# Kernel optimization log

Measured on AMD Instinct MI355X. Metric: run time of the kernel, lower is better.

The kernel has to match this reference:

```python
import jax, jax.numpy as jnp
import numpy as np

N_NODES = 100000
N_EDGES = 1600000
DIM = 128
N_LAYERS = 3
BN_EPS = 1e-5


def setup_inputs() -> dict:
    key = jax.random.key(0)
    ks = jax.random.split(key, 8)
    x = jax.random.normal(ks[0], (N_NODES, DIM), dtype=jnp.float32)
    edge_index = jax.random.randint(ks[1], (2, N_EDGES), 0, N_NODES, dtype=jnp.int64)
    batch = jax.random.randint(ks[2], (N_NODES,), 0, 64, dtype=jnp.int64)
    # stacked per-layer params (input_dim == hidden_dim == 128)
    W = jax.random.normal(ks[3], (N_LAYERS, DIM, DIM), dtype=jnp.float32) / np.sqrt(DIM)
    b = jnp.zeros((N_LAYERS, DIM), dtype=jnp.float32)
    gamma = jax.random.normal(ks[4], (N_LAYERS, DIM), dtype=jnp.float32) * 0.1 + 1.0
    beta = jax.random.normal(ks[5], (N_LAYERS, DIM), dtype=jnp.float32) * 0.1
    running_mean = jax.random.normal(ks[6], (N_LAYERS, DIM), dtype=jnp.float32) * 0.1
    running_var = jax.random.uniform(ks[7], (N_LAYERS, DIM), dtype=jnp.float32, minval=0.5, maxval=1.5)
    return {"x": x, "edge_index": edge_index, "batch": batch, "W": W, "b": b,
            "gamma": gamma, "beta": beta,
            "running_mean": running_mean, "running_var": running_var}


def reference(x, edge_index, batch, W, b, gamma, beta, running_mean, running_var):
    # batch is unused by the original forward (kept for signature fidelity)
    n = x.shape[0]
    # GCNConv adds self-loops once per layer; precompute augmented edge list + norm
    loops = jnp.arange(n, dtype=edge_index.dtype)
    src = jnp.concatenate([edge_index[0], loops])
    dst = jnp.concatenate([edge_index[1], loops])
    deg = jax.ops.segment_sum(jnp.ones_like(dst, dtype=x.dtype), dst, num_segments=n)
    dinv = jax.lax.rsqrt(jnp.maximum(deg, 1e-12))
    norm = dinv[src] * dinv[dst]  # [E+N]

    h = x
    for l in range(N_LAYERS):
        # GCNConv: propagate normalized messages of (h @ W), then add bias
        hw = h @ W[l]                                   # [N, D]
        msg = hw[src] * norm[:, None]                   # gather  [E+N, D]
        h = jax.ops.segment_sum(msg, dst, num_segments=n) + b[l]
        # BatchNorm1d (eval mode: running stats) + ReLU; dropout is identity in eval
        h = gamma[l] * (h - running_mean[l]) * jax.lax.rsqrt(running_var[l] + BN_EPS) + beta[l]
        h = jax.nn.relu(h)
    return h
```

## Files before the change

### kernel.cpp

```cpp
#include <hip/hip_runtime.h>

#define N_NODES 100000
#define N_EDGES 1600000
#define DIM 128
#define BN_EPS 1e-5f
#define BSHIFT 9
#define BN 512
#define NB 196
#define CAP_S 9216
#define CAP_C 10048
#define CHUNK 4096

typedef _Float16 f16;
typedef _Float16 f16x4 __attribute__((ext_vector_type(4)));
typedef _Float16 f16x8 __attribute__((ext_vector_type(8)));
typedef float f32x4 __attribute__((ext_vector_type(4)));


__global__ __launch_bounds__(256) void k_binA(const int* __restrict__ src,
                                              const int* __restrict__ dst,
                                              int* __restrict__ bcnt,
                                              int2* __restrict__ stage) {
  __shared__ int hist[NB];
  __shared__ int lofs[NB];
  __shared__ int lbase[NB];
  __shared__ int lcur[NB];
  __shared__ int scanbuf[256];
  __shared__ int2 buf[CHUNK];
  int t = threadIdx.x;
  for (int i = t; i < NB; i += 256) { hist[i] = 0; lcur[i] = 0; }
  __syncthreads();
  int e0 = blockIdx.x * CHUNK;
  int en = min(CHUNK, N_EDGES - e0);
  for (int i = t; i < en; i += 256) {
    unsigned d = (unsigned)dst[e0 + i];
    unsigned s = (unsigned)src[e0 + i];
    if (d < N_NODES && s < N_NODES) atomicAdd(&hist[d >> BSHIFT], 1);
  }
  __syncthreads();
  scanbuf[t] = (t < NB) ? hist[t] : 0;
  __syncthreads();
  for (int off = 1; off < 256; off <<= 1) {
    int x = (t >= off) ? scanbuf[t - off] : 0;
    __syncthreads();
    scanbuf[t] += x;
    __syncthreads();
  }
  if (t < NB) {
    lofs[t] = scanbuf[t] - hist[t];
    lbase[t] = atomicAdd(&bcnt[t], hist[t]);
  }
  __syncthreads();
  for (int i = t; i < en; i += 256) {
    int d = dst[e0 + i], s = src[e0 + i];
    if ((unsigned)d < N_NODES && (unsigned)s < N_NODES) {
      int b = d >> BSHIFT;
      int r = atomicAdd(&lcur[b], 1);
      buf[lofs[b] + r] = make_int2(d, s);
    }
  }
  __syncthreads();
  int tot = lofs[NB - 1] + hist[NB - 1];
  for (int i = t; i < tot; i += 256) {
    int2 p = buf[i];
    int b = p.x >> BSHIFT;
    int goff = lbase[b] + (i - lofs[b]);
    if (goff < CAP_S) stage[(size_t)b * CAP_S + goff] = p;
  }
}

__global__ __launch_bounds__(512) void k_binB(const int2* __restrict__ stage,
                                              const int* __restrict__ bcnt,
                                              int* __restrict__ rowpack,
                                              int* __restrict__ col) {
  __shared__ int cnt[BN];
  __shared__ int offs[BN];
  __shared__ int lcur[BN];
  __shared__ int sb[BN];
  __shared__ int mp_s;
  __shared__ int colbuf[CAP_C];
  int b = blockIdx.x, t = threadIdx.x;
  int base = b << BSHIFT;
  int nn = min(BN, N_NODES - base);
  int m = min(bcnt[b], CAP_S);
  const int2* seg = stage + (size_t)b * CAP_S;
  cnt[t] = 0; lcur[t] = 0;
  __syncthreads();
  for (int i = t; i < m; i += 512) atomicAdd(&cnt[seg[i].x - base], 1);
  __syncthreads();
  int pcnt = (cnt[t] + 3) & ~3;
  sb[t] = pcnt;
  __syncthreads();
  for (int off = 1; off < 512; off <<= 1) {
    int x = (t >= off) ? sb[t - off] : 0;
    __syncthreads();
    sb[t] += x;
    __syncthreads();
  }
  offs[t] = sb[t] - pcnt;
  if (t == 511) mp_s = sb[511];
  __syncthreads();
  for (int i = t; i < m; i += 512) {
    int2 p = seg[i];
    int dl = p.x - base;
    int r = atomicAdd(&lcur[dl], 1);
    int o = offs[dl] + r;
    if (o < CAP_C) colbuf[o] = p.y;
  }
  __syncthreads();
  {
    int o = offs[t], c = cnt[t], pc = (c + 3) & ~3;
    for (int k = c; k < pc; k++)
      if (o + k < CAP_C) colbuf[o + k] = N_NODES;
  }
  __syncthreads();
  if (t < nn) {
    int o = offs[t], c = cnt[t];
    if (o + ((c + 3) & ~3) > CAP_C) { o = 0; c = 0; }
    rowpack[base + t] = (o << 14) | c;
  }
  int mp = min(mp_s, CAP_C);
  for (int i = t; i < mp; i += 512) col[b * CAP_C + i] = colbuf[i];
}


__global__ __launch_bounds__(256) void k_prep(const float* __restrict__ W,
                                              const float* __restrict__ bb,
                                              const float* __restrict__ gamma,
                                              const float* __restrict__ beta,
                                              const float* __restrict__ mean,
                                              const float* __restrict__ var,
                                              f16* __restrict__ wt,
                                              float* __restrict__ scsh,
                                              f16* __restrict__ hwsA,
                                              f16* __restrict__ hwsB,
                                              int* __restrict__ bcnt) {
  int tg = blockIdx.x * 256 + threadIdx.x;
  if (tg < 3 * DIM * DIM) {
    int l = tg / (DIM * DIM), r = tg % (DIM * DIM);
    int c = r >> 7, k = r & 127;
    wt[tg] = (f16)W[l * DIM * DIM + k * DIM + c];
  }
  if (tg < 384) {
    int l = tg >> 7, c = tg & 127, i = l * DIM + c;
    float sc = gamma[i] * rsqrtf(var[i] + BN_EPS);
    scsh[l * 256 + c] = sc;
    scsh[l * 256 + 128 + c] = sc * (bb[i] - mean[i]) + beta[i];
  }
  if (tg >= 49152 && tg < 49152 + 32) {
    int i = tg - 49152;
    f16x8 z = {};
    f16x8* p = (i < 16) ? (f16x8*)hwsA : (f16x8*)hwsB;
    p[(size_t)N_NODES * 16 + (i & 15)] = z;
  }
  if (tg >= 49184 && tg < 49184 + NB) bcnt[tg - 49184] = 0;
}


__global__ __launch_bounds__(256) void k_gemm0(const float* __restrict__ x,
                                               const f16* __restrict__ wt,
                                               const int* __restrict__ rowpack,
                                               f16* __restrict__ HWS) {
  __shared__ f16x8 Hs[64 * 16];
  __shared__ f16x8 WtS[DIM * 16];
  int t = threadIdx.x;
  int row0 = blockIdx.x * 64;
  const float4* xf = (const float4*)x;
  #pragma unroll
  for (int i = 0; i < 4; i++) {
    int q = t + i * 256;
    int r = q >> 4, s = q & 15;
    int gr = row0 + r; if (gr >= N_NODES) gr = N_NODES - 1;
    float4 u0 = xf[(size_t)gr * 32 + s * 2];
    float4 u1 = xf[(size_t)gr * 32 + s * 2 + 1];
    f16x8 o = {(f16)u0.x, (f16)u0.y, (f16)u0.z, (f16)u0.w,
               (f16)u1.x, (f16)u1.y, (f16)u1.z, (f16)u1.w};
    Hs[r * 16 + (s ^ (r & 7))] = o;
  }
  const f16x8* Wg = (const f16x8*)wt;
  #pragma unroll
  for (int i = 0; i < 8; i++) {
    int q = t + i * 256;
    int c = q >> 4, s = q & 15;
    WtS[c * 16 + (s ^ (c & 7))] = Wg[(size_t)c * 16 + s];
  }
  __syncthreads();

  int wid = t >> 6, l = t & 63;
  int wrow = wid * 16;
  int lr = l & 15, lg = l >> 4;
  int r = wrow + lr, rx = r & 7, rbase = r * 16;
  f16x8 afr[4];
  #pragma unroll
  for (int kk = 0; kk < 4; kk++) afr[kk] = Hs[rbase + ((kk * 4 + lg) ^ rx)];

  f32x4 acc[8] = {};
  #pragma unroll
  for (int ct = 0; ct < 8; ct++) {
    int c = ct * 16 + lr, cx = c & 7, cbase = c * 16;
    #pragma unroll
    for (int kk = 0; kk < 4; kk++) {
      f16x8 bfr = WtS[cbase + ((kk * 4 + lg) ^ cx)];
      acc[ct] = __builtin_amdgcn_mfma_f32_16x16x32_f16(afr[kk], bfr, acc[ct], 0, 0, 0);
    }
  }
  int orow = row0 + wrow + lg * 4;
  #pragma unroll
  for (int i = 0; i < 4; i++) {
    int gr = orow + i;
    if (gr < N_NODES) {
      float dv = rsqrtf((float)(rowpack[gr] & 0x3FFF) + 1.0f);
      #pragma unroll
      for (int ct = 0; ct < 8; ct++)
        HWS[(size_t)gr * DIM + ct * 16 + lr] = (f16)(acc[ct][i] * dv);
    }
  }
}


__global__ __launch_bounds__(256) void k_fused(const f16* __restrict__ hwsIn,
                                               const f16* __restrict__ wt,
                                               const int* __restrict__ rowpack,
                                               const int* __restrict__ col,
                                               const float* __restrict__ scsh,
                                               f16* __restrict__ hwsOut) {
  __shared__ f16x8 Hs[64 * 16];
  int t = threadIdx.x;
  int row = t >> 2;
  int qd = t & 3;
  int n = blockIdx.x * 64 + row;
  int rp = (n < N_NODES) ? rowpack[n] : 0;
  int deg = rp & 0x3FFF, off = rp >> 14;
  int pdeg = (deg + 3) & ~3;
  int beg = (n >> BSHIFT) * CAP_C + off;
  int selfrow = (n < N_NODES) ? n : N_NODES;
  const f16x8* h8 = (const f16x8*)hwsIn;

  size_t sbs = (size_t)selfrow * 16 + qd * 4;
  f16x8 aA0 = h8[sbs], aA1 = h8[sbs + 1], aA2 = h8[sbs + 2], aA3 = h8[sbs + 3];
  f16x8 aB0 = {}, aB1 = {}, aB2 = {}, aB3 = {};
  for (int j = 0; j + 2 <= pdeg; j += 2) {
    int2 c2 = *(const int2*)(col + beg + j);
    size_t b0 = (size_t)c2.x * 16 + qd * 4;
    size_t b1 = (size_t)c2.y * 16 + qd * 4;
    f16x8 v0 = h8[b0], v1 = h8[b0 + 1], v2 = h8[b0 + 2], v3 = h8[b0 + 3];
    f16x8 w0 = h8[b1], w1 = h8[b1 + 1], w2 = h8[b1 + 2], w3 = h8[b1 + 3];
    aA0 += v0; aA1 += v1; aA2 += v2; aA3 += v3;
    aB0 += w0; aB1 += w1; aB2 += w2; aB3 += w3;
  }
  aA0 += aB0; aA1 += aB1; aA2 += aB2; aA3 += aB3;

  float di = rsqrtf((float)(deg + 1));
  const f32x4* scv = (const f32x4*)scsh;
  const f32x4* shv = (const f32x4*)(scsh + 128);
  f16x8 accs[4] = {aA0, aA1, aA2, aA3};
  #pragma unroll
  for (int k = 0; k < 4; k++) {
    int s = qd * 4 + k;
    f32x4 sc0 = scv[s * 2], sh0 = shv[s * 2];
    f32x4 sc1 = scv[s * 2 + 1], sh1 = shv[s * 2 + 1];
    f16x8 o;
    #pragma unroll
    for (int i = 0; i < 4; i++)
      o[i] = (f16)fmaxf(fmaf((float)accs[k][i] * di, sc0[i], sh0[i]), 0.f);
    #pragma unroll
    for (int i = 0; i < 4; i++)
      o[4 + i] = (f16)fmaxf(fmaf((float)accs[k][4 + i] * di, sc1[i], sh1[i]), 0.f);
    Hs[row * 16 + (s ^ (row & 7))] = o;
  }
  __syncthreads();

  int wid = t >> 6, l = t & 63;
  int wrow = wid * 16;
  int lr = l & 15, lg = l >> 4;
  int r = wrow + lr, rx = r & 7, rbase = r * 16;
  f16x8 afr[4];
  #pragma unroll
  for (int kk = 0; kk < 4; kk++) afr[kk] = Hs[rbase + ((kk * 4 + lg) ^ rx)];

  const f16x8* Wg = (const f16x8*)wt;
  f32x4 acc[8] = {};
  #pragma unroll
  for (int ct = 0; ct < 8; ct++) {
    int c = ct * 16 + lr;
    #pragma unroll
    for (int kk = 0; kk < 4; kk++) {
      f16x8 bfr = Wg[(size_t)c * 16 + kk * 4 + lg];
      acc[ct] = __builtin_amdgcn_mfma_f32_16x16x32_f16(afr[kk], bfr, acc[ct], 0, 0, 0);
    }
  }
  int row0 = blockIdx.x * 64;
  int orow = row0 + wrow + lg * 4;
  #pragma unroll
  for (int i = 0; i < 4; i++) {
    int gr = orow + i;
    if (gr < N_NODES) {
      float dv = rsqrtf((float)(rowpack[gr] & 0x3FFF) + 1.0f);
      #pragma unroll
      for (int ct = 0; ct < 8; ct++)
        hwsOut[(size_t)gr * DIM + ct * 16 + lr] = (f16)(acc[ct][i] * dv);
    }
  }
}


__global__ __launch_bounds__(256) void k_gatherout(const f16* __restrict__ HWS,
                                                   const int* __restrict__ rowpack,
                                                   const int* __restrict__ col,
                                                   const float* __restrict__ scsh,
                                                   float* __restrict__ outF) {
  int tid = blockIdx.x * 256 + threadIdx.x;
  int wid = tid >> 4;
  int cs = tid & 15;
  if (wid >= N_NODES) return;
  int rp = rowpack[wid];
  int deg = rp & 0x3FFF;
  int off = rp >> 14;
  int pdeg = (deg + 3) & ~3;
  int beg = (wid >> BSHIFT) * CAP_C + off;
  const f16x8* h8 = (const f16x8*)HWS;

  f16x8 a0 = h8[(size_t)wid * 16 + cs];
  f16x8 a1 = {}, a2 = {}, a3 = {};
  int j = 0;
  for (; j + 8 <= pdeg; j += 8) {
    int4 c0 = *(const int4*)(col + beg + j);
    int4 c1 = *(const int4*)(col + beg + j + 4);
    f16x8 v0 = h8[(size_t)c0.x * 16 + cs];
    f16x8 v1 = h8[(size_t)c0.y * 16 + cs];
    f16x8 v2 = h8[(size_t)c0.z * 16 + cs];
    f16x8 v3 = h8[(size_t)c0.w * 16 + cs];
    f16x8 v4 = h8[(size_t)c1.x * 16 + cs];
    f16x8 v5 = h8[(size_t)c1.y * 16 + cs];
    f16x8 v6 = h8[(size_t)c1.z * 16 + cs];
    f16x8 v7 = h8[(size_t)c1.w * 16 + cs];
    a0 += v0; a1 += v1; a2 += v2; a3 += v3;
    a0 += v4; a1 += v5; a2 += v6; a3 += v7;
  }
  if (j < pdeg) {
    int4 c0 = *(const int4*)(col + beg + j);
    f16x8 v0 = h8[(size_t)c0.x * 16 + cs];
    f16x8 v1 = h8[(size_t)c0.y * 16 + cs];
    f16x8 v2 = h8[(size_t)c0.z * 16 + cs];
    f16x8 v3 = h8[(size_t)c0.w * 16 + cs];
    a0 += v0; a1 += v1; a2 += v2; a3 += v3;
  }
  a0 += a1; a2 += a3; a0 += a2;

  float di = rsqrtf((float)(deg + 1));
  int c4 = cs * 2;
  const f32x4* scv = (const f32x4*)scsh;
  const f32x4* shv = (const f32x4*)(scsh + 128);
  float o[8];
  #pragma unroll
  for (int half = 0; half < 2; half++) {
    f32x4 sc = scv[c4 + half], sh = shv[c4 + half];
    #pragma unroll
    for (int i = 0; i < 4; i++) {
      float v = (float)a0[half * 4 + i] * di;
      o[half * 4 + i] = fmaxf(fmaf(v, sc[i], sh[i]), 0.f);
    }
  }
  f32x4* of = (f32x4*)outF;
  f32x4 lo = {o[0], o[1], o[2], o[3]}, hi = {o[4], o[5], o[6], o[7]};
  of[(size_t)wid * 32 + c4] = lo;
  of[(size_t)wid * 32 + c4 + 1] = hi;
}


extern "C" void kernel_launch(void* const* d_in, const int* in_sizes, int n_in,
                              void* d_out, int out_size, void* d_ws, size_t ws_size,
                              hipStream_t stream) {
  const float* x = (const float*)d_in[0];
  const int* ei = (const int*)d_in[1];
  const int* srcv = ei;
  const int* dstv = ei + N_EDGES;
  const float* W     = (const float*)d_in[3];
  const float* b     = (const float*)d_in[4];
  const float* gamma = (const float*)d_in[5];
  const float* beta  = (const float*)d_in[6];
  const float* rmean = (const float*)d_in[7];
  const float* rvar  = (const float*)d_in[8];
  float* out = (float*)d_out;

  const size_t off_rowpack = 0;
  const size_t off_col     = 400128;
  const size_t off_scsh    = 400128 + 7877632;
  const size_t off_wt      = off_scsh + 3072;
  const size_t off_hwsB    = off_wt + 98304;
  const size_t off_hwsA    = off_hwsB + 25600256;
  const size_t need = off_hwsA + 25600256;
  if (ws_size < need) return;

  char* ws = (char*)d_ws;
  int*   rowpack = (int*)(ws + off_rowpack);
  int*   col     = (int*)(ws + off_col);
  float* scsh    = (float*)(ws + off_scsh);
  f16*   wt      = (f16*)(ws + off_wt);
  f16*   hwsB    = (f16*)(ws + off_hwsB);
  f16*   hwsA    = (f16*)(ws + off_hwsA);
  int2*  stage   = (int2*)(ws + off_hwsB);
  int*   bcnt    = (int*)(ws + off_hwsA);

  k_prep<<<193, 256, 0, stream>>>(W, b, gamma, beta, rmean, rvar,
                                  wt, scsh, hwsA, hwsB, bcnt);
  k_binA<<<(N_EDGES + CHUNK - 1) / CHUNK, 256, 0, stream>>>(srcv, dstv, bcnt, stage);
  k_binB<<<NB, 512, 0, stream>>>(stage, bcnt, rowpack, col);

  k_gemm0<<<1563, 256, 0, stream>>>(x, wt, rowpack, hwsA);
  k_fused<<<1563, 256, 0, stream>>>(hwsA, wt + DIM * DIM, rowpack, col,
                                    scsh, hwsB);
  k_fused<<<1563, 256, 0, stream>>>(hwsB, wt + 2 * DIM * DIM, rowpack, col,
                                    scsh + 256, hwsA);
  k_gatherout<<<6250, 256, 0, stream>>>(hwsA, rowpack, col, scsh + 512, out);
}
```

Before: 321.1 us.

## Split fused gather+GEMM into separate gather and LDS-staged GEMM kernels

```diff
diff --git a/kernel.cpp b/kernel.cpp
--- a/kernel.cpp
+++ b/kernel.cpp
@@ -132,8 +132,7 @@
                                               const float* __restrict__ var,
                                               f16* __restrict__ wt,
                                               float* __restrict__ scsh,
-                                              f16* __restrict__ hwsA,
-                                              f16* __restrict__ hwsB,
+                                              f16* __restrict__ hws,
                                               int* __restrict__ bcnt) {
   int tg = blockIdx.x * 256 + threadIdx.x;
   if (tg < 3 * DIM * DIM) {
@@ -147,11 +146,9 @@
     scsh[l * 256 + c] = sc;
     scsh[l * 256 + 128 + c] = sc * (bb[i] - mean[i]) + beta[i];
   }
-  if (tg >= 49152 && tg < 49152 + 32) {
-    int i = tg - 49152;
+  if (tg >= 49152 && tg < 49152 + 16) {
     f16x8 z = {};
-    f16x8* p = (i < 16) ? (f16x8*)hwsA : (f16x8*)hwsB;
-    p[(size_t)N_NODES * 16 + (i & 15)] = z;
+    ((f16x8*)hws)[(size_t)N_NODES * 16 + (tg - 49152)] = z;
   }
   if (tg >= 49184 && tg < 49184 + NB) bcnt[tg - 49184] = 0;
 }
@@ -218,55 +215,29 @@
 }
 
 
-__global__ __launch_bounds__(256) void k_fused(const f16* __restrict__ hwsIn,
-                                               const f16* __restrict__ wt,
-                                               const int* __restrict__ rowpack,
-                                               const int* __restrict__ col,
-                                               const float* __restrict__ scsh,
-                                               f16* __restrict__ hwsOut) {
+__global__ __launch_bounds__(256) void k_gemm16(const f16* __restrict__ H16,
+                                                const f16* __restrict__ wt,
+                                                const int* __restrict__ rowpack,
+                                                f16* __restrict__ HWS) {
   __shared__ f16x8 Hs[64 * 16];
+  __shared__ f16x8 WtS[DIM * 16];
   int t = threadIdx.x;
-  int row = t >> 2;
-  int qd = t & 3;
-  int n = blockIdx.x * 64 + row;
-  int rp = (n < N_NODES) ? rowpack[n] : 0;
-  int deg = rp & 0x3FFF, off = rp >> 14;
-  int pdeg = (deg + 3) & ~3;
-  int beg = (n >> BSHIFT) * CAP_C + off;
-  int selfrow = (n < N_NODES) ? n : N_NODES;
-  const f16x8* h8 = (const f16x8*)hwsIn;
-
-  size_t sbs = (size_t)selfrow * 16 + qd * 4;
-  f16x8 aA0 = h8[sbs], aA1 = h8[sbs + 1], aA2 = h8[sbs + 2], aA3 = h8[sbs + 3];
-  f16x8 aB0 = {}, aB1 = {}, aB2 = {}, aB3 = {};
-  for (int j = 0; j + 2 <= pdeg; j += 2) {
-    int2 c2 = *(const int2*)(col + beg + j);
-    size_t b0 = (size_t)c2.x * 16 + qd * 4;
-    size_t b1 = (size_t)c2.y * 16 + qd * 4;
-    f16x8 v0 = h8[b0], v1 = h8[b0 + 1], v2 = h8[b0 + 2], v3 = h8[b0 + 3];
-    f16x8 w0 = h8[b1], w1 = h8[b1 + 1], w2 = h8[b1 + 2], w3 = h8[b1 + 3];
-    aA0 += v0; aA1 += v1; aA2 += v2; aA3 += v3;
-    aB0 += w0; aB1 += w1; aB2 += w2; aB3 += w3;
-  }
-  aA0 += aB0; aA1 += aB1; aA2 += aB2; aA3 += aB3;
-
-  float di = rsqrtf((float)(deg + 1));
-  const f32x4* scv = (const f32x4*)scsh;
-  const f32x4* shv = (const f32x4*)(scsh + 128);
-  f16x8 accs[4] = {aA0, aA1, aA2, aA3};
-  #pragma unroll
-  for (int k = 0; k < 4; k++) {
-    int s = qd * 4 + k;
-    f32x4 sc0 = scv[s * 2], sh0 = shv[s * 2];
-    f32x4 sc1 = scv[s * 2 + 1], sh1 = shv[s * 2 + 1];
-    f16x8 o;
-    #pragma unroll
-    for (int i = 0; i < 4; i++)
-      o[i] = (f16)fmaxf(fmaf((float)accs[k][i] * di, sc0[i], sh0[i]), 0.f);
-    #pragma unroll
-    for (int i = 0; i < 4; i++)
-      o[4 + i] = (f16)fmaxf(fmaf((float)accs[k][4 + i] * di, sc1[i], sh1[i]), 0.f);
-    Hs[row * 16 + (s ^ (row & 7))] = o;
+  int row0 = blockIdx.x * 64;
+
+  const f16x8* Hg = (const f16x8*)H16;
+  #pragma unroll
+  for (int i = 0; i < 4; i++) {
+    int q = t + i * 256;
+    int r = q >> 4, s = q & 15;
+    int gr = row0 + r; if (gr >= N_NODES) gr = N_NODES - 1;
+    Hs[r * 16 + (s ^ (r & 7))] = Hg[(size_t)gr * 16 + s];
+  }
+  const f16x8* Wg = (const f16x8*)wt;
+  #pragma unroll
+  for (int i = 0; i < 8; i++) {
+    int q = t + i * 256;
+    int c = q >> 4, s = q & 15;
+    WtS[c * 16 + (s ^ (c & 7))] = Wg[(size_t)c * 16 + s];
   }
   __syncthreads();
 
@@ -278,18 +249,16 @@
   #pragma unroll
   for (int kk = 0; kk < 4; kk++) afr[kk] = Hs[rbase + ((kk * 4 + lg) ^ rx)];
 
-  const f16x8* Wg = (const f16x8*)wt;
   f32x4 acc[8] = {};
   #pragma unroll
   for (int ct = 0; ct < 8; ct++) {
-    int c = ct * 16 + lr;
+    int c = ct * 16 + lr, cx = c & 7, cbase = c * 16;
     #pragma unroll
     for (int kk = 0; kk < 4; kk++) {
-      f16x8 bfr = Wg[(size_t)c * 16 + kk * 4 + lg];
+      f16x8 bfr = WtS[cbase + ((kk * 4 + lg) ^ cx)];
       acc[ct] = __builtin_amdgcn_mfma_f32_16x16x32_f16(afr[kk], bfr, acc[ct], 0, 0, 0);
     }
   }
-  int row0 = blockIdx.x * 64;
   int orow = row0 + wrow + lg * 4;
   #pragma unroll
   for (int i = 0; i < 4; i++) {
@@ -298,17 +267,19 @@
       float dv = rsqrtf((float)(rowpack[gr] & 0x3FFF) + 1.0f);
       #pragma unroll
       for (int ct = 0; ct < 8; ct++)
-        hwsOut[(size_t)gr * DIM + ct * 16 + lr] = (f16)(acc[ct][i] * dv);
-    }
-  }
-}
-
-
-__global__ __launch_bounds__(256) void k_gatherout(const f16* __restrict__ HWS,
-                                                   const int* __restrict__ rowpack,
-                                                   const int* __restrict__ col,
-                                                   const float* __restrict__ scsh,
-                                                   float* __restrict__ outF) {
+        HWS[(size_t)gr * DIM + ct * 16 + lr] = (f16)(acc[ct][i] * dv);
+    }
+  }
+}
+
+
+__global__ __launch_bounds__(256) void k_gather16(const f16* __restrict__ HWS,
+                                                  const int* __restrict__ rowpack,
+                                                  const int* __restrict__ col,
+                                                  const float* __restrict__ scsh,
+                                                  float* __restrict__ outF,
+                                                  f16* __restrict__ outH,
+                                                  int last) {
   int tid = blockIdx.x * 256 + threadIdx.x;
   int wid = tid >> 4;
   int cs = tid & 15;
@@ -323,7 +294,33 @@
   f16x8 a0 = h8[(size_t)wid * 16 + cs];
   f16x8 a1 = {}, a2 = {}, a3 = {};
   int j = 0;
-  for (; j + 8 <= pdeg; j += 8) {
+  for (; j + 16 <= pdeg; j += 16) {
+    int4 c0 = *(const int4*)(col + beg + j);
+    int4 c1 = *(const int4*)(col + beg + j + 4);
+    int4 c2 = *(const int4*)(col + beg + j + 8);
+    int4 c3 = *(const int4*)(col + beg + j + 12);
+    f16x8 v0 = h8[(size_t)c0.x * 16 + cs];
+    f16x8 v1 = h8[(size_t)c0.y * 16 + cs];
+    f16x8 v2 = h8[(size_t)c0.z * 16 + cs];
+    f16x8 v3 = h8[(size_t)c0.w * 16 + cs];
+    f16x8 v4 = h8[(size_t)c1.x * 16 + cs];
+    f16x8 v5 = h8[(size_t)c1.y * 16 + cs];
+    f16x8 v6 = h8[(size_t)c1.z * 16 + cs];
+    f16x8 v7 = h8[(size_t)c1.w * 16 + cs];
+    f16x8 v8 = h8[(size_t)c2.x * 16 + cs];
+    f16x8 v9 = h8[(size_t)c2.y * 16 + cs];
+    f16x8 va = h8[(size_t)c2.z * 16 + cs];
+    f16x8 vb = h8[(size_t)c2.w * 16 + cs];
+    f16x8 vc = h8[(size_t)c3.x * 16 + cs];
+    f16x8 vd = h8[(size_t)c3.y * 16 + cs];
+    f16x8 ve = h8[(size_t)c3.z * 16 + cs];
+    f16x8 vf = h8[(size_t)c3.w * 16 + cs];
+    a0 += v0; a1 += v1; a2 += v2; a3 += v3;
+    a0 += v4; a1 += v5; a2 += v6; a3 += v7;
+    a0 += v8; a1 += v9; a2 += va; a3 += vb;
+    a0 += vc; a1 += vd; a2 += ve; a3 += vf;
+  }
+  if (j + 8 <= pdeg) {
     int4 c0 = *(const int4*)(col + beg + j);
     int4 c1 = *(const int4*)(col + beg + j + 4);
     f16x8 v0 = h8[(size_t)c0.x * 16 + cs];
@@ -336,6 +333,7 @@
     f16x8 v7 = h8[(size_t)c1.w * 16 + cs];
     a0 += v0; a1 += v1; a2 += v2; a3 += v3;
     a0 += v4; a1 += v5; a2 += v6; a3 += v7;
+    j += 8;
   }
   if (j < pdeg) {
     int4 c0 = *(const int4*)(col + beg + j);
@@ -361,10 +359,16 @@
       o[half * 4 + i] = fmaxf(fmaf(v, sc[i], sh[i]), 0.f);
     }
   }
-  f32x4* of = (f32x4*)outF;
-  f32x4 lo = {o[0], o[1], o[2], o[3]}, hi = {o[4], o[5], o[6], o[7]};
-  of[(size_t)wid * 32 + c4] = lo;
-  of[(size_t)wid * 32 + c4 + 1] = hi;
+  if (last) {
+    f32x4* of = (f32x4*)outF;
+    f32x4 lo = {o[0], o[1], o[2], o[3]}, hi = {o[4], o[5], o[6], o[7]};
+    of[(size_t)wid * 32 + c4] = lo;
+    of[(size_t)wid * 32 + c4 + 1] = hi;
+  } else {
+    f16x8 oh = {(f16)o[0], (f16)o[1], (f16)o[2], (f16)o[3],
+                (f16)o[4], (f16)o[5], (f16)o[6], (f16)o[7]};
+    ((f16x8*)outH)[(size_t)wid * 16 + cs] = oh;
+  }
 }
 
 
@@ -387,9 +391,9 @@
   const size_t off_col     = 400128;
   const size_t off_scsh    = 400128 + 7877632;
   const size_t off_wt      = off_scsh + 3072;
-  const size_t off_hwsB    = off_wt + 98304;
-  const size_t off_hwsA    = off_hwsB + 25600256;
-  const size_t need = off_hwsA + 25600256;
+  const size_t off_h16     = off_wt + 98304;
+  const size_t off_hws     = off_h16 + 25600000;
+  const size_t need = off_hws + 25600256;
   if (ws_size < need) return;
 
   char* ws = (char*)d_ws;
@@ -397,20 +401,19 @@
   int*   col     = (int*)(ws + off_col);
   float* scsh    = (float*)(ws + off_scsh);
   f16*   wt      = (f16*)(ws + off_wt);
-  f16*   hwsB    = (f16*)(ws + off_hwsB);
-  f16*   hwsA    = (f16*)(ws + off_hwsA);
-  int2*  stage   = (int2*)(ws + off_hwsB);
-  int*   bcnt    = (int*)(ws + off_hwsA);
-
-  k_prep<<<193, 256, 0, stream>>>(W, b, gamma, beta, rmean, rvar,
-                                  wt, scsh, hwsA, hwsB, bcnt);
+  f16*   h16     = (f16*)(ws + off_h16);
+  f16*   hws     = (f16*)(ws + off_hws);
+  int2*  stage   = (int2*)(ws + off_h16);
+  int*   bcnt    = (int*)(ws + off_hws);
+
+  k_prep<<<193, 256, 0, stream>>>(W, b, gamma, beta, rmean, rvar, wt, scsh, hws, bcnt);
   k_binA<<<(N_EDGES + CHUNK - 1) / CHUNK, 256, 0, stream>>>(srcv, dstv, bcnt, stage);
   k_binB<<<NB, 512, 0, stream>>>(stage, bcnt, rowpack, col);
 
-  k_gemm0<<<1563, 256, 0, stream>>>(x, wt, rowpack, hwsA);
-  k_fused<<<1563, 256, 0, stream>>>(hwsA, wt + DIM * DIM, rowpack, col,
-                                    scsh, hwsB);
-  k_fused<<<1563, 256, 0, stream>>>(hwsB, wt + 2 * DIM * DIM, rowpack, col,
-                                    scsh + 256, hwsA);
-  k_gatherout<<<6250, 256, 0, stream>>>(hwsA, rowpack, col, scsh + 512, out);
-}
+  k_gemm0<<<1563, 256, 0, stream>>>(x, wt, rowpack, hws);
+  k_gather16<<<6250, 256, 0, stream>>>(hws, rowpack, col, scsh, out, h16, 0);
+  k_gemm16<<<1563, 256, 0, stream>>>(h16, wt + DIM * DIM, rowpack, hws);
+  k_gather16<<<6250, 256, 0, stream>>>(hws, rowpack, col, scsh + 256, out, h16, 0);
+  k_gemm16<<<1563, 256, 0, stream>>>(h16, wt + 2 * DIM * DIM, rowpack, hws);
+  k_gather16<<<6250, 256, 0, stream>>>(hws, rowpack, col, scsh + 512, out, h16, 1);
+}
```

New measurement: 271.0 us. -15.6%, faster.
